# Performance work log

Hardware: AMD Instinct MI355X
Metric: run time of the kernel (lower is better)

The kernel has to match this reference:

```python
import jax, jax.numpy as jnp
import numpy as np

DIM = 512
HEADS = 8
DIM_HEAD = 64
INNER = HEADS * DIM_HEAD  # 512
SCALE = DIM_HEAD ** -0.5


def layer_norm(x, w, b, eps=1e-5):
    mu = jnp.mean(x, axis=-1, keepdims=True)
    var = jnp.var(x, axis=-1, keepdims=True)
    return (x - mu) * jax.lax.rsqrt(var + eps) * w + b


def setup_inputs() -> dict:
    key = jax.random.key(0)
    ks = jax.random.split(key, 8)
    b, n = 8, 1024
    img = jax.random.normal(ks[0], (b, n, DIM), dtype=jnp.float32)
    tab = jax.random.normal(ks[1], (b, 1, DIM), dtype=jnp.float32)
    # params (fan-in scaled)
    w_qkv = jax.random.normal(ks[2], (DIM, 3 * INNER), dtype=jnp.float32) / np.sqrt(DIM)
    w_tab_qkv = jax.random.normal(ks[3], (DIM, 3 * INNER), dtype=jnp.float32) / np.sqrt(DIM)
    w_out = jax.random.normal(ks[4], (INNER, DIM), dtype=jnp.float32) / np.sqrt(INNER)
    b_out = jax.random.normal(ks[5], (DIM,), dtype=jnp.float32) * 0.01
    ln_w = jnp.ones((DIM,), dtype=jnp.float32)
    ln_b = jnp.zeros((DIM,), dtype=jnp.float32)
    return {"img": img, "tab": tab, "w_qkv": w_qkv, "w_tab_qkv": w_tab_qkv,
            "w_out": w_out, "b_out": b_out, "ln_w": ln_w, "ln_b": ln_b}


def reference(img, tab, w_qkv, w_tab_qkv, w_out, b_out, ln_w, ln_b):
    b, n, _ = img.shape
    x = layer_norm(img, ln_w, ln_b)
    qkv = x @ w_qkv  # [b, n, 3*inner]
    q, k, v = jnp.split(qkv, 3, axis=-1)

    def to_heads(t, s):
        return t.reshape(b, s, HEADS, DIM_HEAD).transpose(0, 2, 1, 3)  # [b,h,s,d]

    q, k, v = to_heads(q, n), to_heads(k, n), to_heads(v, n)

    t = layer_norm(tab, ln_w, ln_b)
    qkv_t = t @ w_tab_qkv  # [b, 1, 3*inner]
    _, k_t, v_t = jnp.split(qkv_t, 3, axis=-1)
    k = jnp.concatenate([k, to_heads(k_t, 1)], axis=2)  # [b,h,n+1,d]
    v = jnp.concatenate([v, to_heads(v_t, 1)], axis=2)

    dots = jnp.einsum('bhqd,bhkd->bhqk', q, k) * SCALE  # [b,h,n,n+1]
    attn = jax.nn.softmax(dots, axis=-1)
    out = jnp.einsum('bhqk,bhkd->bhqd', attn, v)
    out = out.transpose(0, 2, 1, 3).reshape(b, n, INNER)
    return out @ w_out + b_out
```

## Files before the change

### kernel.cpp

```cpp
#include <hip/hip_runtime.h>


typedef __attribute__((ext_vector_type(4))) float f32x4;
typedef __attribute__((ext_vector_type(16))) float f32x16;
typedef __attribute__((ext_vector_type(8))) short bf16x8;
typedef __attribute__((ext_vector_type(8))) unsigned short u16x8;

#define MFMA16(a, b, c) __builtin_amdgcn_mfma_f32_16x16x32_bf16(a, b, c, 0, 0, 0)
#define MFMA32(a, b, c) __builtin_amdgcn_mfma_f32_32x32x16_bf16(a, b, c, 0, 0, 0)

#define GLD16(gsrc, ldst)                                                     \
  __builtin_amdgcn_global_load_lds(                                           \
      (const __attribute__((address_space(1))) void*)(gsrc),                  \
      (__attribute__((address_space(3))) void*)(ldst), 16, 0, 0)

#define KPAD 1088

#define QSCALE 0.18033688011112042f

__device__ __forceinline__ unsigned short f2bf(float f) {
  union { float f; unsigned int u; } c; c.f = f;
  unsigned int u = c.u;
  u += 0x7fffu + ((u >> 16) & 1u);
  return (unsigned short)(u >> 16);
}

__device__ __forceinline__ unsigned int cvtpk_bf16(float lo, float hi) {
  unsigned int r;
  asm("v_cvt_pk_bf16_f32 %0, %1, %2" : "=v"(r) : "v"(lo), "v"(hi));
  return r;
}

__global__ __launch_bounds__(256) void k_pre(const float* __restrict__ img,
                                             const float* __restrict__ tab,
                                             const float* __restrict__ w_qkv,
                                             const float* __restrict__ w_tab,
                                             const float* __restrict__ w_out,
                                             const float* __restrict__ ln_w,
                                             const float* __restrict__ ln_b,
                                             unsigned short* __restrict__ x_bf,
                                             unsigned short* __restrict__ wqt,
                                             unsigned short* __restrict__ wot,
                                             unsigned short* __restrict__ kh,
                                             unsigned short* __restrict__ vt) {
  int blk = blockIdx.x, tid = threadIdx.x;
  if (blk < 256) {
    __shared__ unsigned short tbuf[64][68];
    const float* src;
    unsigned short* dst;
    int k0, n0, ldin;
    if (blk < 192) {
      int ti = blk / 24, tj = blk % 24;
      k0 = ti * 64; n0 = tj * 64; ldin = 1536;
      src = w_qkv; dst = wqt;
    } else {
      int g = blk - 192;
      int ti = g >> 3, tj = g & 7;
      k0 = ti * 64; n0 = tj * 64; ldin = 512;
      src = w_out; dst = wot;
    }
    int rr = tid >> 4, c4 = (tid & 15) * 4;
    #pragma unroll
    for (int i = 0; i < 4; ++i) {
      int r = i * 16 + rr;
      float4 v = *(const float4*)(src + (size_t)(k0 + r) * ldin + n0 + c4);
      tbuf[c4 + 0][r] = f2bf(v.x);
      tbuf[c4 + 1][r] = f2bf(v.y);
      tbuf[c4 + 2][r] = f2bf(v.z);
      tbuf[c4 + 3][r] = f2bf(v.w);
    }
    __syncthreads();
    #pragma unroll
    for (int i = 0; i < 4; ++i) {
      int r = i * 16 + rr;
      ushort4 w = *(const ushort4*)&tbuf[r][c4];
      *(ushort4*)(dst + (size_t)(n0 + r) * 512 + k0 + c4) = w;
    }
  } else if (blk < 2304) {
    int wid = tid >> 6, lane = tid & 63;
    int row = (blk - 256) * 4 + wid;
    const float* src = img + (size_t)row * 512;
    float4 v0 = *(const float4*)(src + lane * 8);
    float4 v1 = *(const float4*)(src + lane * 8 + 4);
    float x[8] = {v0.x, v0.y, v0.z, v0.w, v1.x, v1.y, v1.z, v1.w};
    float s = 0.f, sq = 0.f;
    #pragma unroll
    for (int j = 0; j < 8; ++j) { s += x[j]; sq += x[j] * x[j]; }
    #pragma unroll
    for (int off = 32; off >= 1; off >>= 1) {
      s  += __shfl_xor(s, off);
      sq += __shfl_xor(sq, off);
    }
    float mean = s * (1.0f / 512.0f);
    float var  = sq * (1.0f / 512.0f) - mean * mean;
    float rs = rsqrtf(var + 1e-5f);
    float4 w0 = *(const float4*)(ln_w + lane * 8);
    float4 w1 = *(const float4*)(ln_w + lane * 8 + 4);
    float4 b0 = *(const float4*)(ln_b + lane * 8);
    float4 b1 = *(const float4*)(ln_b + lane * 8 + 4);
    float w[8] = {w0.x, w0.y, w0.z, w0.w, w1.x, w1.y, w1.z, w1.w};
    float bb[8] = {b0.x, b0.y, b0.z, b0.w, b1.x, b1.y, b1.z, b1.w};
    bf16x8 o;
    #pragma unroll
    for (int j = 0; j < 8; ++j)
      o[j] = (short)f2bf((x[j] - mean) * rs * w[j] + bb[j]);
    *(bf16x8*)(x_bf + (size_t)row * 512 + lane * 8) = o;
  } else {
    __shared__ float tl[512];
    __shared__ float red[4][64];
    __shared__ float ws_[4], wq_[4];
    int blk2 = blk - 2304;
    int b = blk2 >> 4, chunk = blk2 & 15;
    int t = tid;
    int lane = t & 63, wid = t >> 6;
    int cl = t & 63;
    int ks = t >> 6;
    int col = chunk * 64 + cl;

    {
      int h = chunk & 7;
      int bh = b * 8 + h;
      u16x8 z = (u16x8)(0);
      if (chunk < 8) {
        unsigned short* base = kh + ((size_t)bh * KPAD + 1024) * 64;
        #pragma unroll
        for (int i = 0; i < 2; ++i)
          *(u16x8*)(base + (t + i * 256) * 8) = z;
      } else {
        #pragma unroll
        for (int i = 0; i < 2; ++i) {
          int idx = t + i * 256;
          int d = idx >> 3, ch = idx & 7;
          *(u16x8*)(vt + ((size_t)bh * 64 + d) * KPAD + 1024 + ch * 8) = z;
        }
      }
    }

    float2 tv = *(const float2*)(tab + (size_t)b * 512 + t * 2);
    float s_ = tv.x + tv.y, q_ = tv.x * tv.x + tv.y * tv.y;
    #pragma unroll
    for (int off = 32; off >= 1; off >>= 1) {
      s_ += __shfl_xor(s_, off);
      q_ += __shfl_xor(q_, off);
    }
    if (lane == 0) { ws_[wid] = s_; wq_[wid] = q_; }
    __syncthreads();
    float S = ws_[0] + ws_[1] + ws_[2] + ws_[3];
    float Qq = wq_[0] + wq_[1] + wq_[2] + wq_[3];
    float mean = S * (1.0f / 512.0f);
    float var = Qq * (1.0f / 512.0f) - mean * mean;
    float rs = rsqrtf(var + 1e-5f);
    tl[t * 2 + 0] = (tv.x - mean) * rs * ln_w[t * 2 + 0] + ln_b[t * 2 + 0];
    tl[t * 2 + 1] = (tv.y - mean) * rs * ln_w[t * 2 + 1] + ln_b[t * 2 + 1];
    __syncthreads();

    const float* wp = w_tab + 512 + col + (size_t)(ks * 128) * 1536;
    float s = 0.f;
    #pragma unroll 8
    for (int k = 0; k < 128; ++k)
      s += tl[ks * 128 + k] * wp[(size_t)k * 1536];
    red[ks][cl] = s;
    __syncthreads();
    if (ks == 0) {
      float v = red[0][cl] + red[1][cl] + red[2][cl] + red[3][cl];
      int part = col >> 9, hd = col & 511, h = hd >> 6, d = hd & 63;
      int bh = b * 8 + h;
      unsigned short hv = f2bf(v);
      if (part == 0) kh[((size_t)bh * KPAD + 1024) * 64 + d] = hv;
      else           vt[((size_t)bh * 64 + d) * KPAD + 1024] = hv;
    }
  }
}

__global__ __launch_bounds__(512, 6) void k_qkv(const unsigned short* __restrict__ x_bf,
                                                const unsigned short* __restrict__ wqt,
                                                unsigned short* __restrict__ qh,
                                                unsigned short* __restrict__ kh,
                                                unsigned short* __restrict__ vt) {
  __shared__ unsigned short As[3][128 * 32];
  __shared__ unsigned short Bs[3][128 * 32];
  int tid = threadIdx.x;
  int wid = tid >> 6, lane = tid & 63;
  int bm = blockIdx.x & 63, bn = blockIdx.x >> 6;
  int r0 = bm * 128, c0 = bn * 128;
  int lr = lane & 15, lk = (lane >> 4) * 8;
  int wr = (wid >> 2) * 64, wc = (wid & 3) * 32;
  int srow = tid >> 2, scol = (tid & 3) * 8;
  const unsigned short* gA = x_bf + (size_t)(r0 + srow) * 512 + scol;
  const unsigned short* gB = wqt  + (size_t)(c0 + srow) * 512 + scol;
  int ldsoff = tid * 8;

  f32x4 acc[4][2];
  #pragma unroll
  for (int mi = 0; mi < 4; ++mi)
    #pragma unroll
    for (int ni = 0; ni < 2; ++ni)
      acc[mi][ni] = (f32x4){0.f, 0.f, 0.f, 0.f};

  GLD16(gA,      &As[0][ldsoff]);
  GLD16(gB,      &Bs[0][ldsoff]);
  GLD16(gA + 32, &As[1][ldsoff]);
  GLD16(gB + 32, &Bs[1][ldsoff]);

  int cur = 0, pre = 2;
  for (int t = 0; t < 16; ++t) {
    if (t < 15) asm volatile("s_waitcnt vmcnt(2)" ::: "memory");
    else        asm volatile("s_waitcnt vmcnt(0)" ::: "memory");
    __builtin_amdgcn_s_barrier();
    if (t < 14) {
      int k2 = (t + 2) * 32;
      GLD16(gA + k2, &As[pre][ldsoff]);
      GLD16(gB + k2, &Bs[pre][ldsoff]);
    }
    bf16x8 af[4], bfr[2];
    #pragma unroll
    for (int mi = 0; mi < 4; ++mi)
      af[mi] = *(const bf16x8*)&As[cur][(wr + mi * 16 + lr) * 32 + lk];
    #pragma unroll
    for (int ni = 0; ni < 2; ++ni)
      bfr[ni] = *(const bf16x8*)&Bs[cur][(wc + ni * 16 + lr) * 32 + lk];
    __builtin_amdgcn_s_setprio(1);
    #pragma unroll
    for (int mi = 0; mi < 4; ++mi)
      #pragma unroll
      for (int ni = 0; ni < 2; ++ni)
        acc[mi][ni] = MFMA16(af[mi], bfr[ni], acc[mi][ni]);
    __builtin_amdgcn_s_setprio(0);
    cur = (cur == 2) ? 0 : cur + 1;
    pre = (pre == 2) ? 0 : pre + 1;
  }

  #pragma unroll
  for (int ni = 0; ni < 2; ++ni) {
    int col0 = c0 + wc + ni * 16;
    int which = col0 >> 9;
    int hh = (col0 & 511) >> 6;
    int d = (col0 & 63) + lr;
    #pragma unroll
    for (int mi = 0; mi < 4; ++mi)
      #pragma unroll
      for (int reg = 0; reg < 4; ++reg) {
        int row = r0 + wr + mi * 16 + (lane >> 4) * 4 + reg;
        int b = row >> 10, n = row & 1023;
        int bh = b * 8 + hh;
        float v = acc[mi][ni][reg];
        if (which == 0) {
          qh[((size_t)bh * 1024 + n) * 64 + d] = f2bf(v * QSCALE);
        } else if (which == 1) {
          kh[((size_t)bh * KPAD + n) * 64 + d] = f2bf(v);
        } else {
          vt[((size_t)bh * 64 + d) * KPAD + n] = f2bf(v);
        }
      }
  }
}

__global__ __launch_bounds__(512, 4) void k_attn(const unsigned short* __restrict__ qh,
                                                 const unsigned short* __restrict__ kh,
                                                 const unsigned short* __restrict__ vt,
                                                 unsigned short* __restrict__ ao) {
  __shared__ __align__(16) unsigned short Ks[2][4096];
  __shared__ __align__(16) unsigned short Vs[2][4096];
  int tid = threadIdx.x;
  int wid = tid >> 6, lane = tid & 63;
  int bid = blockIdx.x;
  int swz = ((bid & 7) << 5) | (bid >> 3);
  int bh = swz >> 2;
  int q0 = (swz & 3) * 256 + wid * 32;
  int lq = lane & 31, half = lane >> 5;

  const unsigned short* Q  = qh + (size_t)bh * 1024 * 64;
  const unsigned short* Kg = kh + (size_t)bh * KPAD * 64;
  const unsigned short* Vg = vt + (size_t)bh * 64 * KPAD;

  int xr = tid >> 3;
  int xc = (tid & 7) ^ (xr & 7);
  const unsigned short* kg_src = Kg + xr * 64 + xc * 8;
  const unsigned short* vg_src = Vg + (size_t)xr * KPAD + xc * 8;
  unsigned short* kdstA = &Ks[0][wid * 512];
  unsigned short* kdstB = &Ks[1][wid * 512];
  unsigned short* vdstA = &Vs[0][wid * 512];
  unsigned short* vdstB = &Vs[1][wid * 512];

  bf16x8 qf[4];
  const unsigned short* qlane = Q + (size_t)(q0 + lq) * 64 + half * 8;
  #pragma unroll
  for (int dt = 0; dt < 4; ++dt)
    qf[dt] = *(const bf16x8*)(qlane + dt * 16);

  f32x16 o0 = (f32x16)(0.0f), o1 = (f32x16)(0.0f);
  float m = -1e30f, lsum = 0.f;

  GLD16(kg_src, kdstA);
  GLD16(vg_src, vdstA);
  __syncthreads();

  for (int kt = 0; kt < 17; ++kt) {
    int cur = kt & 1;
    if (kt < 16) {
      GLD16(kg_src + (kt + 1) * 4096, cur ? kdstA : kdstB);
      GLD16(vg_src + (kt + 1) * 64,   cur ? vdstA : vdstB);
    }
    const unsigned short* Kb = Ks[cur];
    const unsigned short* Vb = Vs[cur];
    #pragma unroll
    for (int sub = 0; sub < 2; ++sub) {
      int krow = sub * 32 + lq;
      bf16x8 kf[4];
      #pragma unroll
      for (int dt = 0; dt < 4; ++dt) {
        int ch = (half + dt * 2) ^ (krow & 7);
        kf[dt] = *(const bf16x8*)&Kb[krow * 64 + ch * 8];
      }
      f32x16 s = (f32x16)(0.0f);
      __builtin_amdgcn_s_setprio(1);
      #pragma unroll
      for (int dt = 0; dt < 4; ++dt)
        s = MFMA32(kf[dt], qf[dt], s);
      __builtin_amdgcn_s_setprio(0);
      if (kt == 16) {
        if (sub == 0) {
          #pragma unroll
          for (int reg = 0; reg < 16; ++reg) {
            if (reg == 0) { if (half) s[0] = -1e30f; }
            else s[reg] = -1e30f;
          }
        } else {
          #pragma unroll
          for (int reg = 0; reg < 16; ++reg) s[reg] = -1e30f;
        }
      }
      float pmax = s[0];
      #pragma unroll
      for (int reg = 1; reg < 16; ++reg) pmax = fmaxf(pmax, s[reg]);
      pmax = fmaxf(pmax, __shfl_xor(pmax, 32));
      if (!__all(pmax <= m + 8.0f)) {
        float mnew = fmaxf(m, pmax);
        float al = __builtin_amdgcn_exp2f(m - mnew);
        lsum *= al;
        #pragma unroll
        for (int reg = 0; reg < 16; ++reg) { o0[reg] *= al; o1[reg] *= al; }
        m = mnew;
      }
      float p[16];
      float ls = 0.f;
      #pragma unroll
      for (int reg = 0; reg < 16; ++reg) {
        p[reg] = __builtin_amdgcn_exp2f(s[reg] - m);
        ls += p[reg];
      }
      lsum += ls;
      unsigned int c0x0 = cvtpk_bf16(p[0],  p[1]);
      unsigned int c0x1 = cvtpk_bf16(p[2],  p[3]);
      unsigned int c0y0 = cvtpk_bf16(p[4],  p[5]);
      unsigned int c0y1 = cvtpk_bf16(p[6],  p[7]);
      unsigned int c1x0 = cvtpk_bf16(p[8],  p[9]);
      unsigned int c1x1 = cvtpk_bf16(p[10], p[11]);
      unsigned int c1y0 = cvtpk_bf16(p[12], p[13]);
      unsigned int c1y1 = cvtpk_bf16(p[14], p[15]);
      asm volatile("v_permlane32_swap_b32 %0, %1" : "+v"(c0x0), "+v"(c0y0));
      asm volatile("v_permlane32_swap_b32 %0, %1" : "+v"(c0x1), "+v"(c0y1));
      asm volatile("v_permlane32_swap_b32 %0, %1" : "+v"(c1x0), "+v"(c1y0));
      asm volatile("v_permlane32_swap_b32 %0, %1" : "+v"(c1x1), "+v"(c1y1));
      union { unsigned int w[4]; bf16x8 v; } f0, f1;
      f0.w[0] = c0x0; f0.w[1] = c0x1; f0.w[2] = c0y0; f0.w[3] = c0y1;
      f1.w[0] = c1x0; f1.w[1] = c1x1; f1.w[2] = c1y0; f1.w[3] = c1y1;
      int vr0 = lq, vr1 = lq + 32;
      int cb = sub * 4 + half;
      bf16x8 vf0 = *(const bf16x8*)&Vb[vr0 * 64 + ((cb + 0) ^ (vr0 & 7)) * 8];
      bf16x8 vf1 = *(const bf16x8*)&Vb[vr0 * 64 + ((cb + 2) ^ (vr0 & 7)) * 8];
      bf16x8 vf2 = *(const bf16x8*)&Vb[vr1 * 64 + ((cb + 0) ^ (vr1 & 7)) * 8];
      bf16x8 vf3 = *(const bf16x8*)&Vb[vr1 * 64 + ((cb + 2) ^ (vr1 & 7)) * 8];
      __builtin_amdgcn_s_setprio(1);
      o0 = MFMA32(vf0, f0.v, o0);
      o0 = MFMA32(vf1, f1.v, o0);
      o1 = MFMA32(vf2, f0.v, o1);
      o1 = MFMA32(vf3, f1.v, o1);
      __builtin_amdgcn_s_setprio(0);
    }
    __syncthreads();
  }
  lsum += __shfl_xor(lsum, 32);
  float rl = 1.0f / lsum;
  int b = bh >> 3, h = bh & 7;
  unsigned short* aorow = ao + ((size_t)(b * 1024 + q0 + lq)) * 512 + h * 64;
  #pragma unroll
  for (int dt2 = 0; dt2 < 2; ++dt2) {
    #pragma unroll
    for (int g = 0; g < 4; ++g) {
      ushort4 pk;
      float v0 = (dt2 ? o1[4 * g + 0] : o0[4 * g + 0]) * rl;
      float v1 = (dt2 ? o1[4 * g + 1] : o0[4 * g + 1]) * rl;
      float v2 = (dt2 ? o1[4 * g + 2] : o0[4 * g + 2]) * rl;
      float v3 = (dt2 ? o1[4 * g + 3] : o0[4 * g + 3]) * rl;
      pk.x = f2bf(v0); pk.y = f2bf(v1); pk.z = f2bf(v2); pk.w = f2bf(v3);
      *(ushort4*)(aorow + dt2 * 32 + 8 * g + 4 * half) = pk;
    }
  }
}

__global__ __launch_bounds__(512, 6) void k_out(const unsigned short* __restrict__ ao,
                                                const unsigned short* __restrict__ wot,
                                                const float* __restrict__ b_out,
                                                float* __restrict__ out) {
  __shared__ unsigned short As[3][128 * 32];
  __shared__ unsigned short Bs[3][128 * 32];
  int tid = threadIdx.x;
  int wid = tid >> 6, lane = tid & 63;
  int bm = blockIdx.x & 63, bn = blockIdx.x >> 6;
  int r0 = bm * 128, c0 = bn * 128;
  int lr = lane & 15, lk = (lane >> 4) * 8;
  int wr = (wid >> 2) * 64, wc = (wid & 3) * 32;
  int srow = tid >> 2, scol = (tid & 3) * 8;
  const unsigned short* gA = ao  + (size_t)(r0 + srow) * 512 + scol;
  const unsigned short* gB = wot + (size_t)(c0 + srow) * 512 + scol;
  int ldsoff = tid * 8;

  f32x4 acc[4][2];
  #pragma unroll
  for (int mi = 0; mi < 4; ++mi)
    #pragma unroll
    for (int ni = 0; ni < 2; ++ni)
      acc[mi][ni] = (f32x4){0.f, 0.f, 0.f, 0.f};

  GLD16(gA,      &As[0][ldsoff]);
  GLD16(gB,      &Bs[0][ldsoff]);
  GLD16(gA + 32, &As[1][ldsoff]);
  GLD16(gB + 32, &Bs[1][ldsoff]);

  int cur = 0, pre = 2;
  for (int t = 0; t < 16; ++t) {
    if (t < 15) asm volatile("s_waitcnt vmcnt(2)" ::: "memory");
    else        asm volatile("s_waitcnt vmcnt(0)" ::: "memory");
    __builtin_amdgcn_s_barrier();
    if (t < 14) {
      int k2 = (t + 2) * 32;
      GLD16(gA + k2, &As[pre][ldsoff]);
      GLD16(gB + k2, &Bs[pre][ldsoff]);
    }
    bf16x8 af[4], bfr[2];
    #pragma unroll
    for (int mi = 0; mi < 4; ++mi)
      af[mi] = *(const bf16x8*)&As[cur][(wr + mi * 16 + lr) * 32 + lk];
    #pragma unroll
    for (int ni = 0; ni < 2; ++ni)
      bfr[ni] = *(const bf16x8*)&Bs[cur][(wc + ni * 16 + lr) * 32 + lk];
    __builtin_amdgcn_s_setprio(1);
    #pragma unroll
    for (int mi = 0; mi < 4; ++mi)
      #pragma unroll
      for (int ni = 0; ni < 2; ++ni)
        acc[mi][ni] = MFMA16(af[mi], bfr[ni], acc[mi][ni]);
    __builtin_amdgcn_s_setprio(0);
    cur = (cur == 2) ? 0 : cur + 1;
    pre = (pre == 2) ? 0 : pre + 1;
  }

  #pragma unroll
  for (int ni = 0; ni < 2; ++ni) {
    int col = c0 + wc + ni * 16 + lr;
    float bias = b_out[col];
    #pragma unroll
    for (int mi = 0; mi < 4; ++mi)
      #pragma unroll
      for (int reg = 0; reg < 4; ++reg) {
        int row = r0 + wr + mi * 16 + (lane >> 4) * 4 + reg;
        out[(size_t)row * 512 + col] = acc[mi][ni][reg] + bias;
      }
  }
}

extern "C" void kernel_launch(void* const* d_in, const int* in_sizes, int n_in,
                              void* d_out, int out_size, void* d_ws, size_t ws_size,
                              hipStream_t stream) {
  const float* img       = (const float*)d_in[0];
  const float* tab       = (const float*)d_in[1];
  const float* w_qkv     = (const float*)d_in[2];
  const float* w_tab_qkv = (const float*)d_in[3];
  const float* w_out     = (const float*)d_in[4];
  const float* b_out     = (const float*)d_in[5];
  const float* ln_w      = (const float*)d_in[6];
  const float* ln_b      = (const float*)d_in[7];
  char* ws = (char*)d_ws;
  unsigned short* x_bf = (unsigned short*)(ws);
  unsigned short* wqt  = (unsigned short*)(ws + 8388608);
  unsigned short* wot  = (unsigned short*)(ws + 9961472);
  unsigned short* qh   = (unsigned short*)(ws + 10485760);
  unsigned short* kh   = (unsigned short*)(ws + 18874368);
  unsigned short* vt   = (unsigned short*)(ws + 27787264);
  unsigned short* ao   = (unsigned short*)(ws + 36700160);
  float* out = (float*)d_out;

  hipLaunchKernelGGL(k_pre,  dim3(2432), dim3(256), 0, stream,
                     img, tab, w_qkv, w_tab_qkv, w_out, ln_w, ln_b,
                     x_bf, wqt, wot, kh, vt);
  hipLaunchKernelGGL(k_qkv,  dim3(768),  dim3(512), 0, stream, x_bf, wqt, qh, kh, vt);
  hipLaunchKernelGGL(k_attn, dim3(256),  dim3(512), 0, stream, qh, kh, vt, ao);
  hipLaunchKernelGGL(k_out,  dim3(256),  dim3(512), 0, stream, ao, wot, b_out, out);
}
```

Baseline: 82.51 us.

## Enlarge QKV GEMM tiles to 256x256 with swizzled LDS and double buffering

```diff
diff --git a/kernel.cpp b/kernel.cpp
--- a/kernel.cpp
+++ b/kernel.cpp
@@ -172,72 +172,94 @@
   }
 }
 
-__global__ __launch_bounds__(512, 6) void k_qkv(const unsigned short* __restrict__ x_bf,
+__global__ __launch_bounds__(512, 2) void k_qkv(const unsigned short* __restrict__ x_bf,
                                                 const unsigned short* __restrict__ wqt,
                                                 unsigned short* __restrict__ qh,
                                                 unsigned short* __restrict__ kh,
                                                 unsigned short* __restrict__ vt) {
-  __shared__ unsigned short As[3][128 * 32];
-  __shared__ unsigned short Bs[3][128 * 32];
+  __shared__ unsigned short As[2][256 * 64];
+  __shared__ unsigned short Bs[2][256 * 64];
   int tid = threadIdx.x;
   int wid = tid >> 6, lane = tid & 63;
-  int bm = blockIdx.x & 63, bn = blockIdx.x >> 6;
-  int r0 = bm * 128, c0 = bn * 128;
-  int lr = lane & 15, lk = (lane >> 4) * 8;
-  int wr = (wid >> 2) * 64, wc = (wid & 3) * 32;
-  int srow = tid >> 2, scol = (tid & 3) * 8;
-  const unsigned short* gA = x_bf + (size_t)(r0 + srow) * 512 + scol;
-  const unsigned short* gB = wqt  + (size_t)(c0 + srow) * 512 + scol;
-  int ldsoff = tid * 8;
-
-  f32x4 acc[4][2];
-  #pragma unroll
-  for (int mi = 0; mi < 4; ++mi)
-    #pragma unroll
-    for (int ni = 0; ni < 2; ++ni)
+  int bm = blockIdx.x & 31, bn = blockIdx.x >> 5;
+  int r0 = bm * 256, c0 = bn * 256;
+  int lr = lane & 15, hc = lane >> 4;
+  int wr = (wid >> 2) * 128, wc = (wid & 3) * 64;
+
+  int srowA[4], scA[4];
+  #pragma unroll
+  for (int i = 0; i < 4; ++i) {
+    int id = i * 512 + tid;
+    srowA[i] = id >> 3;
+    scA[i] = (id & 7) ^ (srowA[i] & 7);
+  }
+
+  f32x4 acc[8][4];
+  #pragma unroll
+  for (int mi = 0; mi < 8; ++mi)
+    #pragma unroll
+    for (int ni = 0; ni < 4; ++ni)
       acc[mi][ni] = (f32x4){0.f, 0.f, 0.f, 0.f};
 
-  GLD16(gA,      &As[0][ldsoff]);
-  GLD16(gB,      &Bs[0][ldsoff]);
-  GLD16(gA + 32, &As[1][ldsoff]);
-  GLD16(gB + 32, &Bs[1][ldsoff]);
-
-  int cur = 0, pre = 2;
-  for (int t = 0; t < 16; ++t) {
-    if (t < 15) asm volatile("s_waitcnt vmcnt(2)" ::: "memory");
-    else        asm volatile("s_waitcnt vmcnt(0)" ::: "memory");
+  #define STAGE_QKV(kt, buf)                                                   \
+    do {                                                                       \
+      int kb = (kt) * 64;                                                      \
+      _Pragma("unroll")                                                        \
+      for (int i = 0; i < 4; ++i)                                              \
+        GLD16(x_bf + (size_t)(r0 + srowA[i]) * 512 + kb + scA[i] * 8,          \
+              &As[buf][(i * 512 + tid) * 8]);                                  \
+      _Pragma("unroll")                                                        \
+      for (int i = 0; i < 4; ++i)                                              \
+        GLD16(wqt + (size_t)(c0 + srowA[i]) * 512 + kb + scA[i] * 8,           \
+              &Bs[buf][(i * 512 + tid) * 8]);                                  \
+    } while (0)
+
+  STAGE_QKV(0, 0);
+  STAGE_QKV(1, 1);
+
+  for (int t = 0; t < 8; ++t) {
+    int cur = t & 1;
+    if (t < 7) asm volatile("s_waitcnt vmcnt(8)" ::: "memory");
+    else       asm volatile("s_waitcnt vmcnt(0)" ::: "memory");
     __builtin_amdgcn_s_barrier();
-    if (t < 14) {
-      int k2 = (t + 2) * 32;
-      GLD16(gA + k2, &As[pre][ldsoff]);
-      GLD16(gB + k2, &Bs[pre][ldsoff]);
-    }
-    bf16x8 af[4], bfr[2];
-    #pragma unroll
-    for (int mi = 0; mi < 4; ++mi)
-      af[mi] = *(const bf16x8*)&As[cur][(wr + mi * 16 + lr) * 32 + lk];
-    #pragma unroll
-    for (int ni = 0; ni < 2; ++ni)
-      bfr[ni] = *(const bf16x8*)&Bs[cur][(wc + ni * 16 + lr) * 32 + lk];
-    __builtin_amdgcn_s_setprio(1);
-    #pragma unroll
-    for (int mi = 0; mi < 4; ++mi)
-      #pragma unroll
-      for (int ni = 0; ni < 2; ++ni)
-        acc[mi][ni] = MFMA16(af[mi], bfr[ni], acc[mi][ni]);
-    __builtin_amdgcn_s_setprio(0);
-    cur = (cur == 2) ? 0 : cur + 1;
-    pre = (pre == 2) ? 0 : pre + 1;
-  }
-
-  #pragma unroll
-  for (int ni = 0; ni < 2; ++ni) {
+    __builtin_amdgcn_sched_barrier(0);
+    #pragma unroll
+    for (int kk = 0; kk < 2; ++kk) {
+      bf16x8 af[8], bfr[4];
+      #pragma unroll
+      for (int mi = 0; mi < 8; ++mi) {
+        int row = wr + mi * 16 + lr;
+        int q = (kk * 4 + hc) ^ (row & 7);
+        af[mi] = *(const bf16x8*)&As[cur][row * 64 + q * 8];
+      }
+      #pragma unroll
+      for (int ni = 0; ni < 4; ++ni) {
+        int row = wc + ni * 16 + lr;
+        int q = (kk * 4 + hc) ^ (row & 7);
+        bfr[ni] = *(const bf16x8*)&Bs[cur][row * 64 + q * 8];
+      }
+      __builtin_amdgcn_s_setprio(1);
+      #pragma unroll
+      for (int mi = 0; mi < 8; ++mi)
+        #pragma unroll
+        for (int ni = 0; ni < 4; ++ni)
+          acc[mi][ni] = MFMA16(af[mi], bfr[ni], acc[mi][ni]);
+      __builtin_amdgcn_s_setprio(0);
+    }
+    __builtin_amdgcn_s_barrier();
+    __builtin_amdgcn_sched_barrier(0);
+    if (t < 6) STAGE_QKV(t + 2, cur);
+  }
+  #undef STAGE_QKV
+
+  #pragma unroll
+  for (int ni = 0; ni < 4; ++ni) {
     int col0 = c0 + wc + ni * 16;
     int which = col0 >> 9;
     int hh = (col0 & 511) >> 6;
     int d = (col0 & 63) + lr;
     #pragma unroll
-    for (int mi = 0; mi < 4; ++mi)
+    for (int mi = 0; mi < 8; ++mi)
       #pragma unroll
       for (int reg = 0; reg < 4; ++reg) {
         int row = r0 + wr + mi * 16 + (lane >> 4) * 4 + reg;
@@ -494,7 +516,7 @@
   hipLaunchKernelGGL(k_pre,  dim3(2432), dim3(256), 0, stream,
                      img, tab, w_qkv, w_tab_qkv, w_out, ln_w, ln_b,
                      x_bf, wqt, wot, kh, vt);
-  hipLaunchKernelGGL(k_qkv,  dim3(768),  dim3(512), 0, stream, x_bf, wqt, qh, kh, vt);
+  hipLaunchKernelGGL(k_qkv,  dim3(192),  dim3(512), 0, stream, x_bf, wqt, qh, kh, vt);
   hipLaunchKernelGGL(k_attn, dim3(256),  dim3(512), 0, stream, qh, kh, vt, ao);
   hipLaunchKernelGGL(k_out,  dim3(256),  dim3(512), 0, stream, ao, wot, b_out, out);
 }
```

Result: slower. 104.4 us (+26.5%).
